# Performance work log

Measured on AMD Instinct MI355X. Metric: run time of the kernel, lower is better.

The kernel has to match this reference:

```python
import jax, jax.numpy as jnp
import numpy as np

DN = ('NCHW', 'OIHW', 'NCHW')
BN_EPS = 1e-5


def _conv3x3(x, w, b):
    y = jax.lax.conv_general_dilated(x, w, (1, 1), ((1, 1), (1, 1)), dimension_numbers=DN)
    return y + b[None, :, None, None]


def _bn(x, g, b, m, v):
    # eval-mode BatchNorm with running stats
    scale = g * jax.lax.rsqrt(v + BN_EPS)
    return (x - m[None, :, None, None]) * scale[None, :, None, None] + b[None, :, None, None]


def _bilinear_gather(x, py, px):
    # x: [B,C,H,W]; py, px: [B,K,H,W] float sampling coords (zero padding outside)
    B, C, H, W = x.shape
    y0 = jnp.floor(py)
    x0 = jnp.floor(px)
    wy = py - y0
    wx = px - x0
    y0i = y0.astype(jnp.int32)
    x0i = x0.astype(jnp.int32)
    xf = x.reshape(B, C, H * W)

    def corner(yi, xi, wgt):
        valid = (yi >= 0) & (yi < H) & (xi >= 0) & (xi < W)
        idx = jnp.clip(yi, 0, H - 1) * W + jnp.clip(xi, 0, W - 1)  # [B,K,H,W]
        g = jax.vmap(lambda xb, ib: xb[:, ib])(xf, idx)            # [B,C,K,H,W]
        return g * (wgt * valid.astype(x.dtype))[:, None]

    v = corner(y0i, x0i, (1 - wy) * (1 - wx))
    v = v + corner(y0i, x0i + 1, (1 - wy) * wx)
    v = v + corner(y0i + 1, x0i, wy * (1 - wx))
    v = v + corner(y0i + 1, x0i + 1, wy * wx)
    return v  # [B,C,K,H,W]


def _deform_conv(x, offset, mask, w):
    # modulated deformable conv: 3x3, stride 1, pad 1, dilation 1, groups=1, dg=1
    B, C, H, W = x.shape
    K = 9
    ky = jnp.arange(K) // 3 - 1  # kernel row offsets
    kx = jnp.arange(K) % 3 - 1   # kernel col offsets
    dy = offset[:, :K]           # [B,K,H,W]
    dx = offset[:, K:]
    py = dy + (ky[:, None, None] + jnp.arange(H)[None, :, None]).astype(x.dtype)
    px = dx + (kx[:, None, None] + jnp.arange(W)[None, None, :]).astype(x.dtype)
    val = _bilinear_gather(x, py, px) * mask[:, None]  # [B,C,K,H,W]
    O = w.shape[0]
    return jnp.einsum('bckhw,ock->bohw', val, w.reshape(O, C, K))


def _deconv(x, w):
    # ConvTranspose2d k=4 s=2 p=1, bias=False; torch weight layout [Cin, Cout, 4, 4]
    wk = jnp.flip(w, (2, 3)).transpose(1, 0, 2, 3)  # [Cout, Cin, 4, 4]
    return jax.lax.conv_general_dilated(x, wk, (1, 1), ((2, 2), (2, 2)),
                                        lhs_dilation=(2, 2), dimension_numbers=DN)


def setup_inputs() -> dict:
    key = jax.random.key(0)
    ks = jax.random.split(key, 14)
    B, Cin, Cout, H, W = 8, 256, 256, 64, 64
    x = jax.random.normal(ks[0], (B, Cin, H, W), jnp.float32)
    w_off = jax.random.normal(ks[1], (27, Cin, 3, 3), jnp.float32) * 0.01
    b_off = jnp.zeros((27,), jnp.float32)
    w_dcn = jax.random.normal(ks[2], (Cout, Cin, 3, 3), jnp.float32) * (2.0 / (Cin * 9)) ** 0.5
    gamma1 = 1.0 + 0.1 * jax.random.normal(ks[3], (Cout,), jnp.float32)
    beta1 = 0.1 * jax.random.normal(ks[4], (Cout,), jnp.float32)
    mean1 = 0.1 * jax.random.normal(ks[5], (Cout,), jnp.float32)
    var1 = jax.random.uniform(ks[6], (Cout,), jnp.float32, 0.5, 1.5)
    w_up = jax.random.normal(ks[7], (Cout, Cout, 4, 4), jnp.float32) * 0.05
    gamma2 = 1.0 + 0.1 * jax.random.normal(ks[8], (Cout,), jnp.float32)
    beta2 = 0.1 * jax.random.normal(ks[9], (Cout,), jnp.float32)
    mean2 = 0.1 * jax.random.normal(ks[10], (Cout,), jnp.float32)
    var2 = jax.random.uniform(ks[11], (Cout,), jnp.float32, 0.5, 1.5)
    return dict(x=x, w_off=w_off, b_off=b_off, w_dcn=w_dcn,
                gamma1=gamma1, beta1=beta1, mean1=mean1, var1=var1,
                w_up=w_up, gamma2=gamma2, beta2=beta2, mean2=mean2, var2=var2)


def reference(x, w_off, b_off, w_dcn, gamma1, beta1, mean1, var1,
              w_up, gamma2, beta2, mean2, var2):
    offset_mask = _conv3x3(x, w_off, b_off)          # [B,27,H,W]
    ox, oy, m = jnp.split(offset_mask, 3, axis=1)
    offset = jnp.concatenate([ox, oy], axis=1)       # [B,18,H,W]
    mask = jax.nn.sigmoid(m)                         # [B,9,H,W]
    y = _deform_conv(x, offset, mask, w_dcn)
    y = jax.nn.relu(_bn(y, gamma1, beta1, mean1, var1))
    up = _deconv(y, w_up)
    up = jax.nn.relu(_bn(up, gamma2, beta2, mean2, var2))
    return (y, up)
```

## Files before the change

### kernel.cpp

```cpp
#include <hip/hip_runtime.h>
#include <cstddef>


#define B_EPS 1e-5f

typedef __bf16 bf16x8 __attribute__((ext_vector_type(8)));
typedef float f32x4 __attribute__((ext_vector_type(4)));
typedef unsigned short u16;
typedef unsigned int u32;

__device__ __forceinline__ u32 bfr(float f) {
    u32 u = __float_as_uint(f);
    return (u + 0x7FFFu + ((u >> 16) & 1u)) >> 16;
}

__device__ __forceinline__ void gather8(const float* cb2, uint4 q, int g8, f32x4* ga) {
    const float* p00 = cb2 + ((size_t)(q.x & 0xFFFFu) << 5) + g8;
    const float* p01 = cb2 + ((size_t)(q.x >> 16) << 5) + g8;
    const float* p10 = cb2 + ((size_t)(q.y & 0xFFFFu) << 5) + g8;
    const float* p11 = cb2 + ((size_t)(q.y >> 16) << 5) + g8;
    ga[0] = *(const f32x4*)p00; ga[1] = *(const f32x4*)(p00 + 4);
    ga[2] = *(const f32x4*)p01; ga[3] = *(const f32x4*)(p01 + 4);
    ga[4] = *(const f32x4*)p10; ga[5] = *(const f32x4*)(p10 + 4);
    ga[6] = *(const f32x4*)p11; ga[7] = *(const f32x4*)(p11 + 4);
}

__device__ __forceinline__ uint4 packv(uint4 q, const f32x4* ga) {
    const float w00 = __uint_as_float(q.z << 16);
    const float w01 = __uint_as_float(q.z & 0xFFFF0000u);
    const float w10 = __uint_as_float(q.w << 16);
    const float w11 = __uint_as_float(q.w & 0xFFFF0000u);
    union { bf16x8 h; uint4 u; } r;
#pragma unroll
    for (int jj = 0; jj < 4; ++jj) {
        r.h[jj]     = (__bf16)fmaf(w00, ga[0][jj], fmaf(w01, ga[2][jj], fmaf(w10, ga[4][jj], w11 * ga[6][jj])));
        r.h[4 + jj] = (__bf16)fmaf(w00, ga[1][jj], fmaf(w01, ga[3][jj], fmaf(w10, ga[5][jj], w11 * ga[7][jj])));
    }
    return r.u;
}

__global__ __launch_bounds__(256) void k_prep_wdb(const float* __restrict__ w,
                                                  u16* __restrict__ o) {
    int i = blockIdx.x * 256 + threadIdx.x;
    int kk = i & 31; int e = i >> 5;
    int oc = e & 255; int ch = e >> 8;
    int cc = ch & 7; int k = ch >> 3;
    o[i] = (u16)bfr(w[oc * 2304 + (cc * 32 + kk) * 9 + k]);
}

__global__ __launch_bounds__(256) void k_prep_wtb(const float* __restrict__ w,
                                                  u16* __restrict__ o) {
    int i = blockIdx.x * 256 + threadIdx.x;
    int kk = i & 31; int e = i >> 5;
    int oc = e & 255; e >>= 8;
    int cc = e & 31; int cls = e >> 5;
    int tap = kk >> 3, ci = cc * 8 + (kk & 7);
    int ca = cls >> 1, cb = cls & 1;
    int wr = (tap >> 1) ? (ca ? 0 : 1) : (ca ? 2 : 3);
    int wc = (tap & 1) ? (cb ? 0 : 1) : (cb ? 2 : 3);
    o[i] = (u16)bfr(w[ci * 4096 + oc * 16 + wr * 4 + wc]);
}

__global__ __launch_bounds__(256) void k_prep_wob(const float* __restrict__ w,
                                                  u16* __restrict__ o) {
    int i = blockIdx.x * 256 + threadIdx.x;
    int kk = i & 31; int e = i >> 5;
    int oc = e & 31; e >>= 5;
    int part = e & 1; int ch = e >> 1;
    int cc = ch & 7, k = ch >> 3;
    float v = (oc < 27) ? w[oc * 2304 + (cc * 32 + kk) * 9 + k] : 0.f;
    u16 hh = bfr(v);
    if (part) {
        float vh = __uint_as_float((u32)hh << 16);
        hh = (u16)bfr(v - vh);
    }
    o[i] = hh;
}

__global__ __launch_bounds__(256) void k_bn_prep(
    const float* g1, const float* be1, const float* mu1, const float* va1,
    const float* g2, const float* be2, const float* mu2, const float* va2,
    float* bnp) {
    int t = threadIdx.x;
    float s1 = g1[t] * rsqrtf(va1[t] + B_EPS);
    bnp[t] = s1; bnp[256 + t] = be1[t] - mu1[t] * s1;
    float s2 = g2[t] * rsqrtf(va2[t] + B_EPS);
    bnp[512 + t] = s2; bnp[768 + t] = be2[t] - mu2[t] * s2;
}

__global__ __launch_bounds__(256) void k_tr_x(const float* __restrict__ x,
                                              float* __restrict__ xt) {
    const int t = threadIdx.x;
    const int pg = blockIdx.x & 15;
    const int cc = (blockIdx.x >> 4) & 7;
    const int b = blockIdx.x >> 7;
    const int pix = (pg << 8) + t;
    const float* xp = x + ((size_t)b << 20) + ((size_t)(cc << 5) << 12) + pix;
    float v[32];
#pragma unroll
    for (int cl = 0; cl < 32; ++cl) v[cl] = xp[(size_t)cl << 12];
    float* op = xt + ((size_t)b << 20) + ((size_t)cc << 17) + ((size_t)pix << 5);
#pragma unroll
    for (int i = 0; i < 8; ++i)
        *(f32x4*)(op + i * 4) = *(const f32x4*)&v[i * 4];
}

__global__ __launch_bounds__(256) void k_prep_xth(const float* __restrict__ x,
                                                  u16* __restrict__ xo) {
    const int t = threadIdx.x;
    const int blk = blockIdx.x % 18;
    const int ccg = (blockIdx.x / 18) & 7;
    const int b = blockIdx.x / 144;
    const int hp = blk * 256 + t;
    if (hp >= 4356) return;
    const int h = hp / 66, w = hp % 66;
    const size_t PL = 4356u * 8u;
    u16* dh = xo + ((size_t)b * 64 + ccg * 4) * PL + (size_t)hp * 8;
    u16* dl = dh + 32 * PL;
    if (h == 0 || h == 65 || w == 0 || w == 65) {
        uint4 z = make_uint4(0, 0, 0, 0);
#pragma unroll
        for (int j = 0; j < 4; ++j) {
            *(uint4*)(dh + (size_t)j * PL) = z;
            *(uint4*)(dl + (size_t)j * PL) = z;
        }
        return;
    }
    const float* xp = x + ((size_t)b << 20) + ((size_t)(ccg * 32) << 12)
                    + ((h - 1) << 6) + (w - 1);
    u16 vh[32], vl[32];
#pragma unroll
    for (int cl = 0; cl < 32; ++cl) {
        float v = xp[(size_t)cl << 12];
        u16 hh = (u16)bfr(v);
        vh[cl] = hh;
        vl[cl] = (u16)bfr(v - __uint_as_float((u32)hh << 16));
    }
#pragma unroll
    for (int j = 0; j < 4; ++j) {
        *(uint4*)(dh + (size_t)j * PL) = *(const uint4*)&vh[j * 8];
        *(uint4*)(dl + (size_t)j * PL) = *(const uint4*)&vl[j * 8];
    }
}

__global__ __launch_bounds__(256) void k_tr_y(const float* __restrict__ y,
                                              u16* __restrict__ yt) {
    const int t = threadIdx.x;
    const int blk = blockIdx.x % 18;
    const int oc = (blockIdx.x / 18) & 7;
    const int b = blockIdx.x / 144;
    const int hp = blk * 256 + t;
    if (hp >= 4356) return;
    const int h = hp / 66, w = hp % 66;
    u16* dstb = yt + (((size_t)b * 32 + oc * 4) * 4356 + hp) * 8;
    if (h == 0 || h == 65 || w == 0 || w == 65) {
        uint4 z = make_uint4(0, 0, 0, 0);
#pragma unroll
        for (int j = 0; j < 4; ++j)
            *(uint4*)(dstb + (size_t)j * (4356 * 8)) = z;
        return;
    }
    const float* yp = y + ((size_t)b << 20) + ((size_t)(oc * 32) << 12)
                    + ((h - 1) << 6) + (w - 1);
    u16 vv[32];
#pragma unroll
    for (int cl = 0; cl < 32; ++cl) vv[cl] = (u16)bfr(yp[(size_t)cl << 12]);
#pragma unroll
    for (int j = 0; j < 4; ++j)
        *(uint4*)(dstb + (size_t)j * (4356 * 8)) = *(const uint4*)&vv[j * 8];
}

__global__ __launch_bounds__(256, 2) void k_offset_mfma(
    const u16* __restrict__ xth, const u16* __restrict__ Wob,
    const float* __restrict__ b_off, float* __restrict__ om)
{
    __shared__ float sR[4][2048];
    const int t = threadIdx.x;
    const int bid = blockIdx.x;
    const int lid = ((bid & 7) << 6) + (bid >> 3);
    const int h0 = lid & 63;
    const int b = lid >> 6;
    const int wv = t >> 6;
    const int lane = t & 63;
    const int quad = lane >> 4;
    const int ln = lane & 15;
    const size_t PL = 4356u * 8u;
    const u16* xbb = xth + (size_t)b * 64 * PL;

    f32x4 acc[2][4];
#pragma unroll
    for (int i = 0; i < 2; ++i)
#pragma unroll
        for (int j = 0; j < 4; ++j) acc[i][j] = (f32x4)0.f;

#pragma unroll 3
    for (int ci = 0; ci < 18; ++ci) {
        const int ch = wv * 18 + ci;
        const int k = ch >> 3, cc = ch & 7;
        const int dy = k / 3, dx = k - dy * 3;
        const int hp = (h0 + dy) * 66 + dx + ln;
        const u16* Bh = xbb + (size_t)((cc << 2) + quad) * PL + (size_t)hp * 8;
        const u16* Bl = Bh + 32 * PL;
        const u16* Ap = Wob + ch * 2048 + ln * 32 + (quad << 3);
        bf16x8 ah[2], al[2], bh[4], bl[4];
        ah[0] = *(const bf16x8*)(Ap);
        ah[1] = *(const bf16x8*)(Ap + 512);
        al[0] = *(const bf16x8*)(Ap + 1024);
        al[1] = *(const bf16x8*)(Ap + 1536);
#pragma unroll
        for (int ni = 0; ni < 4; ++ni) {
            bh[ni] = *(const bf16x8*)(Bh + ni * 128);
            bl[ni] = *(const bf16x8*)(Bl + ni * 128);
        }
#pragma unroll
        for (int mi = 0; mi < 2; ++mi)
#pragma unroll
            for (int ni = 0; ni < 4; ++ni) {
                acc[mi][ni] = __builtin_amdgcn_mfma_f32_16x16x32_bf16(
                    ah[mi], bh[ni], acc[mi][ni], 0, 0, 0);
                acc[mi][ni] = __builtin_amdgcn_mfma_f32_16x16x32_bf16(
                    al[mi], bh[ni], acc[mi][ni], 0, 0, 0);
                acc[mi][ni] = __builtin_amdgcn_mfma_f32_16x16x32_bf16(
                    ah[mi], bl[ni], acc[mi][ni], 0, 0, 0);
            }
    }

    float* sw = &sR[wv][0];
#pragma unroll
    for (int mi = 0; mi < 2; ++mi)
#pragma unroll
        for (int ni = 0; ni < 4; ++ni)
            *(f32x4*)&sw[((mi << 2) + ni) * 256 + (lane << 2)] = acc[mi][ni];
    __syncthreads();

#pragma unroll
    for (int j = 0; j < 8; ++j) {
        int flat = (t << 3) + j;
        int e = flat >> 8;
        int rem = flat & 255;
        int l2 = rem >> 2, r = rem & 3;
        int co = ((e >> 2) << 4) + ((l2 >> 4) << 2) + r;
        if (co < 27) {
            float s = sR[0][flat] + sR[1][flat] + sR[2][flat] + sR[3][flat];
            int w = ((e & 3) << 4) + (l2 & 15);
            om[(size_t)b * 110592 + ((size_t)co << 12) + (h0 << 6) + w]
                = s + b_off[co];
        }
    }
}

__global__ __launch_bounds__(256) void k_prep_coeff(
    const float* __restrict__ om, uint4* __restrict__ cpk)
{
    int i = blockIdx.x * 256 + threadIdx.x;
    int pix = i & 4095;
    int bk = i >> 12;
    int k = bk % 9;
    int b = bk / 9;
    int h = pix >> 6, w = pix & 63;
    const float* omb = om + (size_t)b * 110592;
    float dy = omb[(k << 12) + pix];
    float dx = omb[((9 + k) << 12) + pix];
    float mr = omb[((18 + k) << 12) + pix];
    float m  = 1.f / (1.f + __expf(-mr));
    float py = dy + (float)(k / 3 - 1 + h);
    float px = dx + (float)(k % 3 - 1 + w);
    float y0f = floorf(py), x0f = floorf(px);
    float wy = py - y0f, wx = px - x0f;
    int y0 = (int)y0f, x0 = (int)x0f;
    int y1 = y0 + 1, x1 = x0 + 1;
    float vy0 = ((unsigned)y0 < 64u) ? 1.f : 0.f;
    float vy1 = ((unsigned)y1 < 64u) ? 1.f : 0.f;
    float vx0 = ((unsigned)x0 < 64u) ? 1.f : 0.f;
    float vx1 = ((unsigned)x1 < 64u) ? 1.f : 0.f;
    int cy0 = min(max(y0, 0), 63), cy1 = min(max(y1, 0), 63);
    int cx0 = min(max(x0, 0), 63), cx1 = min(max(x1, 0), 63);
    u32 xw = (u32)((cy0 << 6) + cx0) | ((u32)((cy0 << 6) + cx1) << 16);
    u32 yw = (u32)((cy1 << 6) + cx0) | ((u32)((cy1 << 6) + cx1) << 16);
    float w00 = m * (1.f - wy) * (1.f - wx) * vy0 * vx0;
    float w01 = m * (1.f - wy) * wx         * vy0 * vx1;
    float w10 = m * wy         * (1.f - wx) * vy1 * vx0;
    float w11 = m * wy         * wx         * vy1 * vx1;
    u32 zw = bfr(w00) | (bfr(w01) << 16);
    u32 ww2 = bfr(w10) | (bfr(w11) << 16);
    cpk[i] = make_uint4(xw, yw, zw, ww2);
}

__global__ __launch_bounds__(256, 2) void k_deform_mfma(
    const float* __restrict__ xt, const u16* __restrict__ Wdb,
    const uint4* __restrict__ cpk, const float* __restrict__ bnp,
    float* __restrict__ yout)
{
    __shared__ __align__(16) u16 sB[2][64 * 40];
    const int t = threadIdx.x;
    const int bid = blockIdx.x;
    const int lid = ((bid & 7) << 6) + (bid >> 3);
    const int row = lid & 63;
    const int b = lid >> 6;
    const int pix0 = row << 6;
    const int p = t >> 2;
    const int g = t & 3;
    const int g8 = g << 3;
    const float* xtb = xt + ((size_t)b << 20);

    const int lane = t & 63;
    const int wv = t >> 6;
    const int quad = lane >> 4;
    const int ln = lane & 15;
    const u16* Wrow = Wdb + (size_t)(wv * 64 + ln) * 32 + quad * 8;

    f32x4 acc[4][4];
#pragma unroll
    for (int i = 0; i < 4; ++i)
#pragma unroll
        for (int j = 0; j < 4; ++j) acc[i][j] = (f32x4)0.f;

    bf16x8 afb[2][4];
    uint4 qcur = cpk[(size_t)(b * 9) * 4096 + pix0 + p];
    {
#pragma unroll
        for (int mi = 0; mi < 4; ++mi)
            afb[0][mi] = *(const bf16x8*)(Wrow + mi * 512);
        f32x4 ga[8];
        gather8(xtb, qcur, g8, ga);
        *(uint4*)&sB[0][p * 40 + g8] = packv(qcur, ga);
        __syncthreads();
    }

    for (int k = 0; k < 9; ++k) {
        uint4 qnext = qcur;
        if (k < 8) qnext = cpk[(size_t)(b * 9 + k + 1) * 4096 + pix0 + p];
#pragma unroll
        for (int cc = 0; cc < 8; ++cc) {
            const int ch = k * 8 + cc;
            const int par = cc & 1;
            const bool pre = ch < 71;
            const uint4 q = (cc == 7) ? qnext : qcur;
            f32x4 ga[8];
            if (pre) {
                const u16* Wn = Wrow + (size_t)(ch + 1) * 8192;
#pragma unroll
                for (int mi = 0; mi < 4; ++mi)
                    afb[par ^ 1][mi] = *(const bf16x8*)(Wn + mi * 512);
                gather8(xtb + ((size_t)((cc + 1) & 7) << 17), q, g8, ga);
            }
            bf16x8 bg[4];
#pragma unroll
            for (int i = 0; i < 4; ++i)
                bg[i] = *(const bf16x8*)&sB[par][(i * 16 + ln) * 40 + quad * 8];
#pragma unroll
            for (int mi = 0; mi < 4; ++mi)
#pragma unroll
                for (int ni = 0; ni < 4; ++ni)
                    acc[mi][ni] = __builtin_amdgcn_mfma_f32_16x16x32_bf16(
                        afb[par][mi], bg[ni], acc[mi][ni], 0, 0, 0);
            if (pre)
                *(uint4*)&sB[par ^ 1][p * 40 + g8] = packv(q, ga);
            __syncthreads();
        }
        qcur = qnext;
    }

    const float* sc1 = bnp;
    const float* bi1 = bnp + 256;
    float* yb2 = yout + ((size_t)b << 20);
#pragma unroll
    for (int mi = 0; mi < 4; ++mi) {
#pragma unroll
        for (int r = 0; r < 4; ++r) {
            int o = wv * 64 + mi * 16 + quad * 4 + r;
            float sc = sc1[o], bi = bi1[o];
#pragma unroll
            for (int ni = 0; ni < 4; ++ni) {
                float v = fmaxf(fmaf(acc[mi][ni][r], sc, bi), 0.f);
                yb2[((size_t)o << 12) + pix0 + ni * 16 + ln] = v;
            }
        }
    }
}

__global__ __launch_bounds__(256, 4) void k_deconv_mfma(
    const u16* __restrict__ yt, const u16* __restrict__ Wtb,
    const float* __restrict__ bnp, float* __restrict__ up)
{
    const int t = threadIdx.x;
    const int bid = blockIdx.x;
    const int b = bid & 7;
    const int local = bid >> 3;
    const int h0 = local >> 2;
    const int cls = local & 3;
    const int ca = cls >> 1, cb = cls & 1;
    const int DH0 = ca ? 0 : -1, DH1 = ca ? 1 : 0;
    const int DW0 = cb ? 0 : -1, DW1 = cb ? 1 : 0;

    const int lane = t & 63;
    const int wv = t >> 6;
    const int quad = lane >> 4;
    const int ln = lane & 15;

    const int DHq = (quad >> 1) ? DH1 : DH0;
    const int DWq = (quad & 1) ? DW1 : DW0;

    const u16* ytb = yt + (size_t)b * (32u * 4356 * 8);
    const u16* Bb[4];
#pragma unroll
    for (int i = 0; i < 4; ++i) {
        int pix = i * 16 + ln;
        Bb[i] = ytb + (size_t)((h0 + DHq + 1) * 66 + (pix + DWq + 1)) * 8;
    }
    const u16* Ab = Wtb + (size_t)(cls * 32) * 8192
                  + (size_t)(wv * 64 + ln) * 32 + quad * 8;

    f32x4 acc[4][4];
#pragma unroll
    for (int i = 0; i < 4; ++i)
#pragma unroll
        for (int j = 0; j < 4; ++j) acc[i][j] = (f32x4)0.f;

    bf16x8 af[2][4], bg[2][4];
#pragma unroll
    for (int mi = 0; mi < 4; ++mi)
        af[0][mi] = *(const bf16x8*)(Ab + mi * 512);
#pragma unroll
    for (int i = 0; i < 4; ++i)
        bg[0][i] = *(const bf16x8*)(Bb[i]);

#pragma unroll 2
    for (int cc = 0; cc < 32; ++cc) {
        const int par = cc & 1;
        if (cc < 31) {
#pragma unroll
            for (int mi = 0; mi < 4; ++mi)
                af[par ^ 1][mi] = *(const bf16x8*)(Ab + (size_t)(cc + 1) * 8192 + mi * 512);
#pragma unroll
            for (int i = 0; i < 4; ++i)
                bg[par ^ 1][i] = *(const bf16x8*)(Bb[i] + (size_t)(cc + 1) * (4356 * 8));
        }
#pragma unroll
        for (int mi = 0; mi < 4; ++mi)
#pragma unroll
            for (int ni = 0; ni < 4; ++ni)
                acc[mi][ni] = __builtin_amdgcn_mfma_f32_16x16x32_bf16(
                    af[par][mi], bg[par][ni], acc[mi][ni], 0, 0, 0);
    }

    const float* sc2 = bnp + 512;
    const float* bi2 = bnp + 768;
    float* ub = up + ((size_t)b << 22);
    const int pr = (h0 << 1) + ca;
#pragma unroll
    for (int mi = 0; mi < 4; ++mi) {
#pragma unroll
        for (int r = 0; r < 4; ++r) {
            int o = wv * 64 + mi * 16 + quad * 4 + r;
            float sc = sc2[o], bi = bi2[o];
#pragma unroll
            for (int ni = 0; ni < 4; ++ni) {
                int qc = ((ni * 16 + ln) << 1) + cb;
                float v = fmaxf(fmaf(acc[mi][ni][r], sc, bi), 0.f);
                ub[((size_t)o << 14) + (pr << 7) + qc] = v;
            }
        }
    }
}

extern "C" void kernel_launch(void* const* d_in, const int* in_sizes, int n_in,
                              void* d_out, int out_size, void* d_ws, size_t ws_size,
                              hipStream_t stream)
{
    const float* x     = (const float*)d_in[0];
    const float* w_off = (const float*)d_in[1];
    const float* b_off = (const float*)d_in[2];
    const float* w_dcn = (const float*)d_in[3];
    const float* g1    = (const float*)d_in[4];
    const float* be1   = (const float*)d_in[5];
    const float* mu1   = (const float*)d_in[6];
    const float* va1   = (const float*)d_in[7];
    const float* w_up  = (const float*)d_in[8];
    const float* g2    = (const float*)d_in[9];
    const float* be2   = (const float*)d_in[10];
    const float* mu2   = (const float*)d_in[11];
    const float* va2   = (const float*)d_in[12];

    float* yout = (float*)d_out;
    float* up   = (float*)d_out + 8388608;
    float* xt   = up;
    u16*   xth  = (u16*)((char*)up + 33554432);

    char* ws = (char*)d_ws;
    float* om    = (float*)(ws + 0);
    uint4* cpk   = (uint4*)(ws + 3787776);
    u16*   Wob   = (u16*)  (ws + 3787776);
    u16*   Wdb   = (u16*)  (ws + 8506368);
    u16*   yt    = (u16*)  (ws + 0);
    u16*   Wtb   = (u16*)  (ws + 17842176);
    float* bnp   = (float*)(ws + 19939328);

    k_prep_wdb  <<<2304, 256, 0, stream>>>(w_dcn, Wdb);
    k_prep_wtb  <<<4096, 256, 0, stream>>>(w_up, Wtb);
    k_prep_wob  <<<576,  256, 0, stream>>>(w_off, Wob);
    k_bn_prep   <<<1,    256, 0, stream>>>(g1, be1, mu1, va1, g2, be2, mu2, va2, bnp);
    k_tr_x      <<<1024, 256, 0, stream>>>(x, xt);
    k_prep_xth  <<<1152, 256, 0, stream>>>(x, xth);
    k_offset_mfma<<<512, 256, 0, stream>>>(xth, Wob, b_off, om);
    k_prep_coeff<<<1152, 256, 0, stream>>>(om, cpk);
    k_deform_mfma<<<512, 256, 0, stream>>>(xt, Wdb, cpk, bnp, yout);
    k_tr_y      <<<1152, 256, 0, stream>>>(yout, yt);
    k_deconv_mfma<<<2048,256, 0, stream>>>(yt, Wtb, bnp, up);
}
```

Baseline: 459.3 us.

## Pair column-parity classes per deconv block for vectorized float2 output stores

Each deconv block now handles both column parities (cb=0 and cb=1) for half the row's pixels, rather than one parity class for all 64 pixels. Adjacent output columns then land in the same thread and are written with a single float2 store instead of two strided scalar stores. The explicit software double-buffering of the A/B fragments is dropped in favour of plain per-iteration loads, which relies on the compiler and occupancy to hide load latency. Each block also loads weight fragments for two classes per channel chunk, so it moves more A data per block.

```diff
diff --git a/kernel.cpp b/kernel.cpp
--- a/kernel.cpp
+++ b/kernel.cpp
@@ -6,6 +6,7 @@
 
 typedef __bf16 bf16x8 __attribute__((ext_vector_type(8)));
 typedef float f32x4 __attribute__((ext_vector_type(4)));
+typedef float f32x2 __attribute__((ext_vector_type(2)));
 typedef unsigned short u16;
 typedef unsigned int u32;
 
@@ -387,11 +388,10 @@
     const int bid = blockIdx.x;
     const int b = bid & 7;
     const int local = bid >> 3;
+    const int chf = local & 1;
+    const int ca = (local >> 1) & 1;
     const int h0 = local >> 2;
-    const int cls = local & 3;
-    const int ca = cls >> 1, cb = cls & 1;
     const int DH0 = ca ? 0 : -1, DH1 = ca ? 1 : 0;
-    const int DW0 = cb ? 0 : -1, DW1 = cb ? 1 : 0;
 
     const int lane = t & 63;
     const int wv = t >> 6;
@@ -399,49 +399,49 @@
     const int ln = lane & 15;
 
     const int DHq = (quad >> 1) ? DH1 : DH0;
-    const int DWq = (quad & 1) ? DW1 : DW0;
+    const int DWq0 = (quad & 1) ? 0 : -1;
 
     const u16* ytb = yt + (size_t)b * (32u * 4356 * 8);
-    const u16* Bb[4];
-#pragma unroll
-    for (int i = 0; i < 4; ++i) {
-        int pix = i * 16 + ln;
-        Bb[i] = ytb + (size_t)((h0 + DHq + 1) * 66 + (pix + DWq + 1)) * 8;
-    }
-    const u16* Ab = Wtb + (size_t)(cls * 32) * 8192
-                  + (size_t)(wv * 64 + ln) * 32 + quad * 8;
+    const u16* Bb[2][2];
+#pragma unroll
+    for (int i = 0; i < 2; ++i) {
+        int P = chf * 32 + i * 16 + ln;
+        int rowb = (h0 + DHq + 1) * 66 + P + DWq0 + 1;
+        Bb[0][i] = ytb + (size_t)rowb * 8;
+        Bb[1][i] = ytb + (size_t)(rowb + 1) * 8;
+    }
+    const u16* Ab0 = Wtb + (size_t)((ca * 2) * 32) * 8192
+                   + (size_t)(wv * 64 + ln) * 32 + quad * 8;
+    const u16* Ab1 = Ab0 + (size_t)32 * 8192;
 
     f32x4 acc[4][4];
 #pragma unroll
     for (int i = 0; i < 4; ++i)
 #pragma unroll
         for (int j = 0; j < 4; ++j) acc[i][j] = (f32x4)0.f;
-
-    bf16x8 af[2][4], bg[2][4];
-#pragma unroll
-    for (int mi = 0; mi < 4; ++mi)
-        af[0][mi] = *(const bf16x8*)(Ab + mi * 512);
-#pragma unroll
-    for (int i = 0; i < 4; ++i)
-        bg[0][i] = *(const bf16x8*)(Bb[i]);
 
 #pragma unroll 2
     for (int cc = 0; cc < 32; ++cc) {
-        const int par = cc & 1;
-        if (cc < 31) {
-#pragma unroll
-            for (int mi = 0; mi < 4; ++mi)
-                af[par ^ 1][mi] = *(const bf16x8*)(Ab + (size_t)(cc + 1) * 8192 + mi * 512);
-#pragma unroll
-            for (int i = 0; i < 4; ++i)
-                bg[par ^ 1][i] = *(const bf16x8*)(Bb[i] + (size_t)(cc + 1) * (4356 * 8));
+        bf16x8 af0[4], af1[4], bg[2][2];
+#pragma unroll
+        for (int mi = 0; mi < 4; ++mi) {
+            af0[mi] = *(const bf16x8*)(Ab0 + (size_t)cc * 8192 + mi * 512);
+            af1[mi] = *(const bf16x8*)(Ab1 + (size_t)cc * 8192 + mi * 512);
+        }
+#pragma unroll
+        for (int i = 0; i < 2; ++i) {
+            bg[0][i] = *(const bf16x8*)(Bb[0][i] + (size_t)cc * (4356 * 8));
+            bg[1][i] = *(const bf16x8*)(Bb[1][i] + (size_t)cc * (4356 * 8));
         }
 #pragma unroll
         for (int mi = 0; mi < 4; ++mi)
 #pragma unroll
-            for (int ni = 0; ni < 4; ++ni)
-                acc[mi][ni] = __builtin_amdgcn_mfma_f32_16x16x32_bf16(
-                    af[par][mi], bg[par][ni], acc[mi][ni], 0, 0, 0);
+            for (int i = 0; i < 2; ++i) {
+                acc[mi][i] = __builtin_amdgcn_mfma_f32_16x16x32_bf16(
+                    af0[mi], bg[0][i], acc[mi][i], 0, 0, 0);
+                acc[mi][2 + i] = __builtin_amdgcn_mfma_f32_16x16x32_bf16(
+                    af1[mi], bg[1][i], acc[mi][2 + i], 0, 0, 0);
+            }
     }
 
     const float* sc2 = bnp + 512;
@@ -455,10 +455,12 @@
             int o = wv * 64 + mi * 16 + quad * 4 + r;
             float sc = sc2[o], bi = bi2[o];
 #pragma unroll
-            for (int ni = 0; ni < 4; ++ni) {
-                int qc = ((ni * 16 + ln) << 1) + cb;
-                float v = fmaxf(fmaf(acc[mi][ni][r], sc, bi), 0.f);
-                ub[((size_t)o << 14) + (pr << 7) + qc] = v;
+            for (int i = 0; i < 2; ++i) {
+                int qc = (chf * 32 + i * 16 + ln) << 1;
+                f32x2 v2;
+                v2[0] = fmaxf(fmaf(acc[mi][i][r], sc, bi), 0.f);
+                v2[1] = fmaxf(fmaf(acc[mi][2 + i][r], sc, bi), 0.f);
+                *(f32x2*)(ub + ((size_t)o << 14) + (pr << 7) + qc) = v2;
             }
         }
     }
```

Measured after the change: 500.6 us. +9.0%, slower.
